# Optimization experiments

Hardware: AMD Instinct MI355X
Metric: run time of the kernel (lower is better)

Reference implementation:

```python
import math
import jax, jax.numpy as jnp
import numpy as np

CAPACITY_FACTOR = 1.0
LOAD_BALANCE_RATIO = 0.01


def setup_inputs() -> dict:
    key = jax.random.key(0)
    k1, k2 = jax.random.split(key)
    x = jax.random.normal(k1, (16384, 4096), dtype=jnp.float32)
    wg = jax.random.normal(k2, (4096, 64), dtype=jnp.float32) * 0.02
    return {"x": x, "wg": wg}


def reference(x, wg):
    # router logits: [S, E]
    logits = jnp.einsum('sd,de->se', x, wg)
    gates = jax.nn.softmax(logits, axis=1)
    S, E = gates.shape
    capacity_fp = max(min(float(S), S / E * CAPACITY_FACTOR), 4.0)
    capacity = math.ceil(capacity_fp)

    # top-1 expert per token
    indices_s = jnp.argmax(gates, axis=1)                  # [S] int
    mask1 = jax.nn.one_hot(indices_s, E, dtype=jnp.int32)  # [S, E]

    # load-balance statistics
    me = jnp.sum(gates, axis=0) / S                        # router prob fraction
    ce = jnp.sum(mask1.astype(jnp.float32), axis=0) / S    # dispatch fraction

    # position of each token within its expert queue
    locations1 = jnp.cumsum(mask1, axis=0) - 1             # [S, E]
    # 'cut' token drop: keep only tokens within capacity
    mask1 = mask1 * (locations1 < capacity).astype(jnp.int32)
    locations1_s = jnp.sum(locations1 * mask1, axis=1)     # [S]
    mask_sum = jnp.sum(mask1, axis=1)                      # [S]

    # dispatch mask: [E, capacity] of token ids (-1 = empty slot)
    token_ids = jnp.arange(S, dtype=jnp.int32)
    dispatch_indices = jnp.where(mask_sum == 0, -1, indices_s * capacity + locations1_s)
    dispatch_mask = jnp.full((E * capacity + 1,), -1, dtype=jnp.int32)
    dispatch_mask = dispatch_mask.at[dispatch_indices].set(token_ids)
    dispatch_mask = dispatch_mask[:-1].reshape(E, capacity)

    # combine weight per token (0 for dropped tokens)
    gates1_s = jnp.sum(gates * mask1.astype(jnp.float32), axis=1).reshape(1, -1)

    # load-balance aux loss (Switch/GShard form) * ratio
    loss = LOAD_BALANCE_RATIO * E * jnp.sum(me * ce)
    return loss, gates1_s, dispatch_mask
```

## Files before the change

### kernel.cpp

```cpp
#include <hip/hip_runtime.h>
#include <math.h>

#define S_TOK 16384
#define DDIM  4096
#define NEXP  64
#define CAP   256
#define NB    256
#define KT    64
#define NKT   (DDIM / KT)

__global__ __launch_bounds__(256) void gemm_gate_kernel(
    const float* __restrict__ x, const float* __restrict__ wg,
    int* __restrict__ arg_idx, float* __restrict__ gateval,
    int* __restrict__ cnt_part, float* __restrict__ gsum_part)
{
    __shared__ float As[KT * 64];
    __shared__ float Bs[KT * 64];
    __shared__ float gsum_sh[NEXP];
    __shared__ int   cnt_sh[NEXP];

    const int t  = threadIdx.x;
    const int tx = t & 15;
    const int ty = t >> 4;
    const int blk   = blockIdx.x;
    const int mBase = blk * 64;

    if (t < NEXP) { gsum_sh[t] = 0.f; cnt_sh[t] = 0; }

    float acc[4][4];
#pragma unroll
    for (int i = 0; i < 4; i++)
#pragma unroll
        for (int j = 0; j < 4; j++) acc[i][j] = 0.f;

    float4 aR[4], bR[4];

    auto loadTile = [&](int kt) {
#pragma unroll
        for (int i = 0; i < 4; i++) {
            int idx = i * 256 + t;
            int m = idx >> 4, kc = idx & 15;
            aR[i] = *reinterpret_cast<const float4*>(
                &x[(size_t)(mBase + m) * DDIM + kt * KT + kc * 4]);
            int r = idx >> 4, ec = idx & 15;
            bR[i] = *reinterpret_cast<const float4*>(
                &wg[(size_t)(kt * KT + r) * NEXP + ec * 4]);
        }
    };

    auto storeTile = [&]() {
#pragma unroll
        for (int i = 0; i < 4; i++) {
            int idx = i * 256 + t;
            int m = idx >> 4, kc = idx & 15;
            *reinterpret_cast<float4*>(
                &As[(kc << 8) + ((m ^ (kc << 2)) << 2)]) = aR[i];
            int r = idx >> 4, ec = idx & 15;
            *reinterpret_cast<float4*>(&Bs[r * 64 + ec * 4]) = bR[i];
        }
    };

    loadTile(0);
    for (int kt = 0; kt < NKT; kt++) {
        __syncthreads();
        storeTile();
        __syncthreads();
        if (kt + 1 < NKT) loadTile(kt + 1);
#pragma unroll
        for (int kg = 0; kg < 16; kg++) {
            float4 af[4], bf[4];
#pragma unroll
            for (int mi = 0; mi < 4; mi++)
                af[mi] = *reinterpret_cast<const float4*>(
                    &As[(kg << 8) + ((((ty << 2) + mi) ^ (kg << 2)) << 2)]);
#pragma unroll
            for (int j = 0; j < 4; j++)
                bf[j] = *reinterpret_cast<const float4*>(
                    &Bs[((kg << 2) + j) * 64 + (tx << 2)]);
#pragma unroll
            for (int j = 0; j < 4; j++) {
                float bv[4] = {bf[j].x, bf[j].y, bf[j].z, bf[j].w};
#pragma unroll
                for (int mi = 0; mi < 4; mi++) {
                    const float av = reinterpret_cast<const float*>(&af[mi])[j];
#pragma unroll
                    for (int ei = 0; ei < 4; ei++)
                        acc[mi][ei] = fmaf(av, bv[ei], acc[mi][ei]);
                }
            }
        }
    }

    float rden[4];
    int   bi[4];
#pragma unroll
    for (int mi = 0; mi < 4; mi++) {
        float m_ = acc[mi][0];
        int   b_ = tx * 4;
#pragma unroll
        for (int ei = 1; ei < 4; ei++) {
            if (acc[mi][ei] > m_) { m_ = acc[mi][ei]; b_ = tx * 4 + ei; }
        }
#pragma unroll
        for (int msk = 1; msk <= 8; msk <<= 1) {
            float om = __shfl_xor(m_, msk, 64);
            int   ob = __shfl_xor(b_, msk, 64);
            if (om > m_ || (om == m_ && ob < b_)) { m_ = om; b_ = ob; }
        }
        bi[mi] = b_;
        float s_ = 0.f;
#pragma unroll
        for (int ei = 0; ei < 4; ei++) {
            acc[mi][ei] = __expf(acc[mi][ei] - m_);
            s_ += acc[mi][ei];
        }
#pragma unroll
        for (int msk = 1; msk <= 8; msk <<= 1) s_ += __shfl_xor(s_, msk, 64);
        rden[mi] = 1.f / s_;
    }

#pragma unroll
    for (int ei = 0; ei < 4; ei++) {
        float c_ = 0.f;
#pragma unroll
        for (int mi = 0; mi < 4; mi++) c_ += acc[mi][ei] * rden[mi];
        c_ += __shfl_xor(c_, 16, 64);
        c_ += __shfl_xor(c_, 32, 64);
        if ((t & 48) == 0) atomicAdd(&gsum_sh[tx * 4 + ei], c_);
    }

    if ((t & 15) == 0) {
#pragma unroll
        for (int mi = 0; mi < 4; mi++) {
            int tok = mBase + ty * 4 + mi;
            arg_idx[tok] = bi[mi];
            gateval[tok] = rden[mi];
            atomicAdd(&cnt_sh[bi[mi]], 1);
        }
    }
    __syncthreads();
    if (t < NEXP) {
        gsum_part[blk * NEXP + t] = gsum_sh[t];
        cnt_part[blk * NEXP + t]  = cnt_sh[t];
    }
}

__global__ __launch_bounds__(256) void scan_kernel(
    const int* __restrict__ cnt_part, const float* __restrict__ gsum_part,
    int* __restrict__ offsets, float* __restrict__ loss_out)
{
    __shared__ int   qs[4][NEXP];
    __shared__ float qg[4][NEXP];
    const int t = threadIdx.x;
    const int e = t & 63, q = t >> 6;

    int   s = 0;
    float g = 0.f;
    for (int i = 0; i < 64; i++) {
        int b = q * 64 + i;
        s += cnt_part[b * NEXP + e];
        g += gsum_part[b * NEXP + e];
    }
    qs[q][e] = s;
    qg[q][e] = g;
    __syncthreads();

    int base = 0;
    for (int q2 = 0; q2 < q; q2++) base += qs[q2][e];
    int run = base;
    for (int i = 0; i < 64; i++) {
        int b = q * 64 + i;
        offsets[b * NEXP + e] = run;
        run += cnt_part[b * NEXP + e];
    }

    if (q == 0) {
        int   totc = qs[0][e] + qs[1][e] + qs[2][e] + qs[3][e];
        float totg = qg[0][e] + qg[1][e] + qg[2][e] + qg[3][e];
        float lp = (totg / (float)S_TOK) * ((float)totc / (float)S_TOK);
#pragma unroll
        for (int msk = 1; msk < 64; msk <<= 1) lp += __shfl_xor(lp, msk, 64);
        if (t == 0) loss_out[0] = 0.01f * (float)NEXP * lp;
    }
}

__global__ __launch_bounds__(64) void dispatch_kernel(
    const int* __restrict__ arg_idx, const float* __restrict__ gateval,
    const int* __restrict__ offsets,
    float* __restrict__ out_gates, float* __restrict__ out_disp)
{
    __shared__ int sh_e[64];
    const int t = threadIdx.x, blk = blockIdx.x;
    const int tok = blk * 64 + t;
    const int e = arg_idx[tok];
    sh_e[t] = e;
    __syncthreads();
    int rank = 0;
    for (int j = 0; j < t; j++) rank += (sh_e[j] == e);
    int loc = offsets[blk * NEXP + e] + rank;
    float gv = 0.f;
    if (loc < CAP) {
        gv = gateval[tok];
        out_disp[e * CAP + loc] = (float)tok;
    }
    out_gates[tok] = gv;
}

__global__ __launch_bounds__(256) void init_kernel(float* __restrict__ out_disp)
{
    int i = blockIdx.x * 256 + threadIdx.x;
    out_disp[i] = -1.0f;
}

extern "C" void kernel_launch(void* const* d_in, const int* in_sizes, int n_in,
                              void* d_out, int out_size, void* d_ws, size_t ws_size,
                              hipStream_t stream)
{
    const float* x  = (const float*)d_in[0];
    const float* wg = (const float*)d_in[1];

    float* out       = (float*)d_out;
    float* out_loss  = out;
    float* out_gates = out + 1;
    float* out_disp  = out + 1 + S_TOK;

    char* ws = (char*)d_ws;
    int*   arg_idx   = (int*)(ws);
    float* gateval   = (float*)(ws + (64 << 10));
    int*   cnt_part  = (int*)(ws + (128 << 10));
    float* gsum_part = (float*)(ws + (192 << 10));
    int*   offsets   = (int*)(ws + (256 << 10));

    hipLaunchKernelGGL(init_kernel, dim3(NEXP * CAP / 256), dim3(256), 0, stream,
                       out_disp);
    hipLaunchKernelGGL(gemm_gate_kernel, dim3(NB), dim3(256), 0, stream,
                       x, wg, arg_idx, gateval, cnt_part, gsum_part);
    hipLaunchKernelGGL(scan_kernel, dim3(1), dim3(256), 0, stream,
                       cnt_part, gsum_part, offsets, out_loss);
    hipLaunchKernelGGL(dispatch_kernel, dim3(NB), dim3(64), 0, stream,
                       arg_idx, gateval, offsets, out_gates, out_disp);
}
```

Baseline: 619.0 us.

## Split-K the router GEMM with larger tiles and separate softmax reduction

Replaces the single fused GEMM+softmax kernel (256 blocks, 64x64 tiles) with a split-K GEMM of 512 blocks using 256x64 tiles and 8x8 register blocking. Partials go to per-split workspace buffers, or are accumulated with atomics when the workspace is too small. A new softmax kernel then sums the partials and computes argmax, gates, counts and gate sums. The aim is to fill more CUs and raise arithmetic intensity on the 64 MB x read. In exchange it adds an extra pass over partial logits of up to 32 MB and one more launch.

Measured after the change: 593.3 us. 4.2% less time.

```diff
diff --git a/kernel.cpp b/kernel.cpp
--- a/kernel.cpp
+++ b/kernel.cpp
@@ -6,163 +6,182 @@
 #define NEXP  64
 #define CAP   256
 #define NB    256
-#define KT    64
-#define NKT   (DDIM / KT)
-
-__global__ __launch_bounds__(256) void gemm_gate_kernel(
+#define TM    256
+#define KT    32
+#define SPLITS 8
+#define KRANGE (DDIM / SPLITS)
+#define NTILE (KRANGE / KT)
+#define MT    (S_TOK / TM)
+#define APAD  260
+
+template <int ATOMIC>
+__global__ __launch_bounds__(256, 2) void gemm_split_kernel(
     const float* __restrict__ x, const float* __restrict__ wg,
+    float* __restrict__ outbuf)
+{
+    __shared__ float AT[KT * APAD];
+    __shared__ float Bs[KT * NEXP];
+
+    const int t   = threadIdx.x;
+    const int ty  = t >> 3;
+    const int tx  = t & 7;
+    const int blk = blockIdx.x;
+    const int m   = blk & (MT - 1);
+    const int s   = blk >> 6;
+    const int mBase = m * TM;
+    const int kBase = s * KRANGE;
+
+    float acc[8][8] = {};
+    float4 av[8], bv0, bv1;
+
+    auto loadRegs = [&](int tile) {
+        const int k0 = kBase + tile * KT;
+#pragma unroll
+        for (int p = 0; p < 8; p++) {
+            int flat = p * 256 + t;
+            int tok = flat >> 3, kf = flat & 7;
+            av[p] = *reinterpret_cast<const float4*>(
+                &x[(size_t)(mBase + tok) * DDIM + k0 + kf * 4]);
+        }
+        int fl0 = t, fl1 = 256 + t;
+        bv0 = *reinterpret_cast<const float4*>(
+            &wg[(size_t)(k0 + (fl0 >> 4)) * NEXP + (fl0 & 15) * 4]);
+        bv1 = *reinterpret_cast<const float4*>(
+            &wg[(size_t)(k0 + (fl1 >> 4)) * NEXP + (fl1 & 15) * 4]);
+    };
+
+    loadRegs(0);
+    for (int tile = 0; tile < NTILE; tile++) {
+        __syncthreads();
+#pragma unroll
+        for (int p = 0; p < 8; p++) {
+            int flat = p * 256 + t;
+            int tok = flat >> 3, kf = flat & 7;
+#pragma unroll
+            for (int j = 0; j < 4; j++)
+                AT[(kf * 4 + j) * APAD + tok] = (&av[p].x)[j];
+        }
+        {
+            int fl0 = t, fl1 = 256 + t;
+            *reinterpret_cast<float4*>(&Bs[(fl0 >> 4) * NEXP + (fl0 & 15) * 4]) = bv0;
+            *reinterpret_cast<float4*>(&Bs[(fl1 >> 4) * NEXP + (fl1 & 15) * 4]) = bv1;
+        }
+        __syncthreads();
+        if (tile + 1 < NTILE) loadRegs(tile + 1);
+#pragma unroll
+        for (int k = 0; k < KT; k++) {
+            float4 a0 = *reinterpret_cast<const float4*>(&AT[k * APAD + ty * 8]);
+            float4 a1 = *reinterpret_cast<const float4*>(&AT[k * APAD + ty * 8 + 4]);
+            float4 b0 = *reinterpret_cast<const float4*>(&Bs[k * NEXP + tx * 8]);
+            float4 b1 = *reinterpret_cast<const float4*>(&Bs[k * NEXP + tx * 8 + 4]);
+            float aa[8] = {a0.x, a0.y, a0.z, a0.w, a1.x, a1.y, a1.z, a1.w};
+            float bb[8] = {b0.x, b0.y, b0.z, b0.w, b1.x, b1.y, b1.z, b1.w};
+#pragma unroll
+            for (int i = 0; i < 8; i++)
+#pragma unroll
+                for (int j = 0; j < 8; j++)
+                    acc[i][j] = fmaf(aa[i], bb[j], acc[i][j]);
+        }
+    }
+
+#pragma unroll
+    for (int i = 0; i < 8; i++) {
+        size_t row = (size_t)(mBase + ty * 8 + i) * NEXP + tx * 8;
+        if (ATOMIC) {
+#pragma unroll
+            for (int j = 0; j < 8; j++) atomicAdd(&outbuf[row + j], acc[i][j]);
+        } else {
+            float* dst = outbuf + (size_t)s * (S_TOK * NEXP) + row;
+            *reinterpret_cast<float4*>(dst) =
+                make_float4(acc[i][0], acc[i][1], acc[i][2], acc[i][3]);
+            *reinterpret_cast<float4*>(dst + 4) =
+                make_float4(acc[i][4], acc[i][5], acc[i][6], acc[i][7]);
+        }
+    }
+}
+
+__global__ __launch_bounds__(256) void softmax_kernel(
+    const float* __restrict__ buf, int nsplits,
     int* __restrict__ arg_idx, float* __restrict__ gateval,
-    int* __restrict__ cnt_part, float* __restrict__ gsum_part)
-{
-    __shared__ float As[KT * 64];
-    __shared__ float Bs[KT * 64];
-    __shared__ float gsum_sh[NEXP];
-    __shared__ int   cnt_sh[NEXP];
-
-    const int t  = threadIdx.x;
-    const int tx = t & 15;
-    const int ty = t >> 4;
-    const int blk   = blockIdx.x;
-    const int mBase = blk * 64;
-
-    if (t < NEXP) { gsum_sh[t] = 0.f; cnt_sh[t] = 0; }
-
-    float acc[4][4];
-#pragma unroll
-    for (int i = 0; i < 4; i++)
-#pragma unroll
-        for (int j = 0; j < 4; j++) acc[i][j] = 0.f;
-
-    float4 aR[4], bR[4];
-
-    auto loadTile = [&](int kt) {
-#pragma unroll
-        for (int i = 0; i < 4; i++) {
-            int idx = i * 256 + t;
-            int m = idx >> 4, kc = idx & 15;
-            aR[i] = *reinterpret_cast<const float4*>(
-                &x[(size_t)(mBase + m) * DDIM + kt * KT + kc * 4]);
-            int r = idx >> 4, ec = idx & 15;
-            bR[i] = *reinterpret_cast<const float4*>(
-                &wg[(size_t)(kt * KT + r) * NEXP + ec * 4]);
-        }
-    };
-
-    auto storeTile = [&]() {
-#pragma unroll
-        for (int i = 0; i < 4; i++) {
-            int idx = i * 256 + t;
-            int m = idx >> 4, kc = idx & 15;
-            *reinterpret_cast<float4*>(
-                &As[(kc << 8) + ((m ^ (kc << 2)) << 2)]) = aR[i];
-            int r = idx >> 4, ec = idx & 15;
-            *reinterpret_cast<float4*>(&Bs[r * 64 + ec * 4]) = bR[i];
-        }
-    };
-
-    loadTile(0);
-    for (int kt = 0; kt < NKT; kt++) {
-        __syncthreads();
-        storeTile();
-        __syncthreads();
-        if (kt + 1 < NKT) loadTile(kt + 1);
-#pragma unroll
-        for (int kg = 0; kg < 16; kg++) {
-            float4 af[4], bf[4];
-#pragma unroll
-            for (int mi = 0; mi < 4; mi++)
-                af[mi] = *reinterpret_cast<const float4*>(
-                    &As[(kg << 8) + ((((ty << 2) + mi) ^ (kg << 2)) << 2)]);
-#pragma unroll
-            for (int j = 0; j < 4; j++)
-                bf[j] = *reinterpret_cast<const float4*>(
-                    &Bs[((kg << 2) + j) * 64 + (tx << 2)]);
-#pragma unroll
-            for (int j = 0; j < 4; j++) {
-                float bv[4] = {bf[j].x, bf[j].y, bf[j].z, bf[j].w};
-#pragma unroll
-                for (int mi = 0; mi < 4; mi++) {
-                    const float av = reinterpret_cast<const float*>(&af[mi])[j];
-#pragma unroll
-                    for (int ei = 0; ei < 4; ei++)
-                        acc[mi][ei] = fmaf(av, bv[ei], acc[mi][ei]);
-                }
-            }
-        }
-    }
-
-    float rden[4];
-    int   bi[4];
-#pragma unroll
-    for (int mi = 0; mi < 4; mi++) {
-        float m_ = acc[mi][0];
-        int   b_ = tx * 4;
-#pragma unroll
-        for (int ei = 1; ei < 4; ei++) {
-            if (acc[mi][ei] > m_) { m_ = acc[mi][ei]; b_ = tx * 4 + ei; }
-        }
-#pragma unroll
-        for (int msk = 1; msk <= 8; msk <<= 1) {
-            float om = __shfl_xor(m_, msk, 64);
-            int   ob = __shfl_xor(b_, msk, 64);
-            if (om > m_ || (om == m_ && ob < b_)) { m_ = om; b_ = ob; }
-        }
-        bi[mi] = b_;
-        float s_ = 0.f;
-#pragma unroll
-        for (int ei = 0; ei < 4; ei++) {
-            acc[mi][ei] = __expf(acc[mi][ei] - m_);
-            s_ += acc[mi][ei];
-        }
-#pragma unroll
-        for (int msk = 1; msk <= 8; msk <<= 1) s_ += __shfl_xor(s_, msk, 64);
-        rden[mi] = 1.f / s_;
-    }
-
-#pragma unroll
-    for (int ei = 0; ei < 4; ei++) {
-        float c_ = 0.f;
-#pragma unroll
-        for (int mi = 0; mi < 4; mi++) c_ += acc[mi][ei] * rden[mi];
-        c_ += __shfl_xor(c_, 16, 64);
-        c_ += __shfl_xor(c_, 32, 64);
-        if ((t & 48) == 0) atomicAdd(&gsum_sh[tx * 4 + ei], c_);
-    }
-
-    if ((t & 15) == 0) {
-#pragma unroll
-        for (int mi = 0; mi < 4; mi++) {
-            int tok = mBase + ty * 4 + mi;
-            arg_idx[tok] = bi[mi];
-            gateval[tok] = rden[mi];
-            atomicAdd(&cnt_sh[bi[mi]], 1);
-        }
-    }
-    __syncthreads();
-    if (t < NEXP) {
-        gsum_part[blk * NEXP + t] = gsum_sh[t];
-        cnt_part[blk * NEXP + t]  = cnt_sh[t];
-    }
+    int* __restrict__ cnt_part, float* __restrict__ gsum_blk)
+{
+    __shared__ int   cnt_sh[4][NEXP];
+    __shared__ float gs_sh[NEXP];
+    const int t = threadIdx.x;
+    const int w = t >> 6, lane = t & 63;
+    const int tok = blockIdx.x * 256 + t;
+
+    if (t < NEXP) gs_sh[t] = 0.f;
+    cnt_sh[w][lane] = 0;
+    __syncthreads();
+
+    float4 r[16];
+    {
+        const float* p = buf + (size_t)tok * NEXP;
+#pragma unroll
+        for (int q = 0; q < 16; q++)
+            r[q] = *reinterpret_cast<const float4*>(p + q * 4);
+    }
+    for (int sp = 1; sp < nsplits; sp++) {
+        const float* ps = buf + (size_t)sp * (S_TOK * NEXP) + (size_t)tok * NEXP;
+#pragma unroll
+        for (int q = 0; q < 16; q++) {
+            float4 v = *reinterpret_cast<const float4*>(ps + q * 4);
+            r[q].x += v.x; r[q].y += v.y; r[q].z += v.z; r[q].w += v.w;
+        }
+    }
+
+    float m_ = r[0].x; int b_ = 0;
+#pragma unroll
+    for (int q = 0; q < 16; q++)
+#pragma unroll
+        for (int j = 0; j < 4; j++) {
+            float v = (&r[q].x)[j];
+            int e = q * 4 + j;
+            if (v > m_) { m_ = v; b_ = e; }
+        }
+
+    float den = 0.f;
+#pragma unroll
+    for (int q = 0; q < 16; q++)
+#pragma unroll
+        for (int j = 0; j < 4; j++) {
+            float g = __expf((&r[q].x)[j] - m_);
+            (&r[q].x)[j] = g;
+            den += g;
+        }
+    float inv = 1.f / den;
+
+    arg_idx[tok] = b_;
+    gateval[tok] = inv;
+    atomicAdd(&cnt_sh[w][b_], 1);
+
+#pragma unroll
+    for (int q = 0; q < 16; q++)
+#pragma unroll
+        for (int j = 0; j < 4; j++) {
+            float v = (&r[q].x)[j] * inv;
+#pragma unroll
+            for (int msk = 1; msk < 64; msk <<= 1) v += __shfl_xor(v, msk, 64);
+            if (lane == 0) atomicAdd(&gs_sh[q * 4 + j], v);
+        }
+
+    __syncthreads();
+    cnt_part[(blockIdx.x * 4 + w) * NEXP + lane] = cnt_sh[w][lane];
+    if (t < NEXP) gsum_blk[blockIdx.x * NEXP + t] = gs_sh[t];
 }
 
 __global__ __launch_bounds__(256) void scan_kernel(
-    const int* __restrict__ cnt_part, const float* __restrict__ gsum_part,
+    const int* __restrict__ cnt_part, const float* __restrict__ gsum_blk,
     int* __restrict__ offsets, float* __restrict__ loss_out)
 {
-    __shared__ int   qs[4][NEXP];
-    __shared__ float qg[4][NEXP];
+    __shared__ int qs[4][NEXP];
     const int t = threadIdx.x;
     const int e = t & 63, q = t >> 6;
 
-    int   s = 0;
-    float g = 0.f;
-    for (int i = 0; i < 64; i++) {
-        int b = q * 64 + i;
-        s += cnt_part[b * NEXP + e];
-        g += gsum_part[b * NEXP + e];
-    }
+    int s = 0;
+    for (int i = 0; i < 64; i++) s += cnt_part[(q * 64 + i) * NEXP + e];
     qs[q][e] = s;
-    qg[q][e] = g;
     __syncthreads();
 
     int base = 0;
@@ -175,8 +194,9 @@
     }
 
     if (q == 0) {
-        int   totc = qs[0][e] + qs[1][e] + qs[2][e] + qs[3][e];
-        float totg = qg[0][e] + qg[1][e] + qg[2][e] + qg[3][e];
+        float totg = 0.f;
+        for (int i = 0; i < 64; i++) totg += gsum_blk[i * NEXP + e];
+        int totc = qs[0][e] + qs[1][e] + qs[2][e] + qs[3][e];
         float lp = (totg / (float)S_TOK) * ((float)totc / (float)S_TOK);
 #pragma unroll
         for (int msk = 1; msk < 64; msk <<= 1) lp += __shfl_xor(lp, msk, 64);
@@ -206,10 +226,17 @@
     out_gates[tok] = gv;
 }
 
-__global__ __launch_bounds__(256) void init_kernel(float* __restrict__ out_disp)
+__global__ __launch_bounds__(256) void init_disp_kernel(float* __restrict__ p)
+{
+    p[blockIdx.x * 256 + threadIdx.x] = -1.0f;
+}
+
+__global__ __launch_bounds__(256) void zero_kernel(float* __restrict__ p, int n4)
 {
     int i = blockIdx.x * 256 + threadIdx.x;
-    out_disp[i] = -1.0f;
+    float4 z = make_float4(0.f, 0.f, 0.f, 0.f);
+    for (; i < n4; i += gridDim.x * 256)
+        reinterpret_cast<float4*>(p)[i] = z;
 }
 
 extern "C" void kernel_launch(void* const* d_in, const int* in_sizes, int n_in,
@@ -225,18 +252,37 @@
     float* out_disp  = out + 1 + S_TOK;
 
     char* ws = (char*)d_ws;
-    int*   arg_idx   = (int*)(ws);
-    float* gateval   = (float*)(ws + (64 << 10));
-    int*   cnt_part  = (int*)(ws + (128 << 10));
-    float* gsum_part = (float*)(ws + (192 << 10));
-    int*   offsets   = (int*)(ws + (256 << 10));
-
-    hipLaunchKernelGGL(init_kernel, dim3(NEXP * CAP / 256), dim3(256), 0, stream,
-                       out_disp);
-    hipLaunchKernelGGL(gemm_gate_kernel, dim3(NB), dim3(256), 0, stream,
-                       x, wg, arg_idx, gateval, cnt_part, gsum_part);
+    int*   arg_idx  = (int*)(ws);
+    float* gateval  = (float*)(ws + (64 << 10));
+    int*   cnt_part = (int*)(ws + (128 << 10));
+    float* gsum_blk = (float*)(ws + (192 << 10));
+    int*   offsets  = (int*)(ws + (208 << 10));
+    float* buf      = (float*)(ws + (512 << 10));
+
+    const size_t splitBytes = (size_t)SPLITS * S_TOK * NEXP * sizeof(float);
+    const bool use_split = ws_size >= (512u << 10) + splitBytes;
+
+    hipLaunchKernelGGL(init_disp_kernel, dim3(NEXP * CAP / 256), dim3(256), 0,
+                       stream, out_disp);
+
+    if (use_split) {
+        hipLaunchKernelGGL((gemm_split_kernel<0>), dim3(MT * SPLITS), dim3(256),
+                           0, stream, x, wg, buf);
+        hipLaunchKernelGGL(softmax_kernel, dim3(S_TOK / 256), dim3(256), 0,
+                           stream, buf, SPLITS, arg_idx, gateval, cnt_part,
+                           gsum_blk);
+    } else {
+        hipLaunchKernelGGL(zero_kernel, dim3(256), dim3(256), 0, stream,
+                           buf, S_TOK * NEXP / 4);
+        hipLaunchKernelGGL((gemm_split_kernel<1>), dim3(MT * SPLITS), dim3(256),
+                           0, stream, x, wg, buf);
+        hipLaunchKernelGGL(softmax_kernel, dim3(S_TOK / 256), dim3(256), 0,
+                           stream, buf, 1, arg_idx, gateval, cnt_part,
+                           gsum_blk);
+    }
+
     hipLaunchKernelGGL(scan_kernel, dim3(1), dim3(256), 0, stream,
-                       cnt_part, gsum_part, offsets, out_loss);
+                       cnt_part, gsum_blk, offsets, out_loss);
     hipLaunchKernelGGL(dispatch_kernel, dim3(NB), dim3(64), 0, stream,
                        arg_idx, gateval, offsets, out_gates, out_disp);
 }
```
